# Kernel tuning notes

Hardware: AMD Instinct MI355X
Metric: run time of the kernel (lower is better)

Reference implementation:

```python
import jax, jax.numpy as jnp
import numpy as np

W = 8          # window_size (small/key side)
WU = 2 * W     # window_size_up (big/query side)
H = 4          # num_heads
SF = 128       # sf_dim
BF = 256       # bf_dim
HD = SF // H   # head_dim = 32
SCALE = HD ** -0.5
TABLE = (2 * WU - 1) * (2 * W - 1)  # 465


def _relative_position_index():
    # big coords (2, WU*WU), small coords (2, W*W), 'ij' meshgrid like torch
    ch, cw = jnp.meshgrid(jnp.arange(WU), jnp.arange(WU), indexing='ij')
    big = jnp.stack([ch.reshape(-1), cw.reshape(-1)])          # (2, Nb)
    sh, sw = jnp.meshgrid(jnp.arange(W), jnp.arange(W), indexing='ij')
    small = jnp.stack([sh.reshape(-1), sw.reshape(-1)])        # (2, Ns)
    rel = big[:, :, None] - small[:, None, :]                  # (2, Nb, Ns)
    idx = (rel[0] + W - 1) * (2 * W - 1) + (rel[1] + W - 1)    # (Nb, Ns)
    return idx


def setup_inputs() -> dict:
    key = jax.random.key(0)
    ks = jax.random.split(key, 9)
    B_ = 1024
    Nb, Ns = WU * WU, W * W
    inp = {
        'big_x': jax.random.normal(ks[0], (B_, Nb, BF), jnp.float32),
        'small_x': jax.random.normal(ks[1], (B_, Ns, SF), jnp.float32),
        # proj1: bf_dim -> sf_dim
        'W1': jax.random.normal(ks[2], (BF, SF), jnp.float32) * (BF ** -0.5),
        'b1': jnp.zeros((SF,), jnp.float32),
        # fused qkv: sf_dim -> 3*sf_dim
        'Wqkv': jax.random.normal(ks[3], (SF, 3 * SF), jnp.float32) * (SF ** -0.5),
        'bqkv': jnp.zeros((3 * SF,), jnp.float32),
        # proj2: sf_dim -> bf_dim
        'W2': jax.random.normal(ks[4], (SF, BF), jnp.float32) * (SF ** -0.5),
        'b2': jnp.zeros((BF,), jnp.float32),
        # relative position bias table, trunc_normal std=0.02
        'bias_table': jax.random.normal(ks[5], (TABLE, H), jnp.float32) * 0.02,
    }
    return inp


def reference(big_x, small_x, W1, b1, Wqkv, bqkv, W2, b2, bias_table):
    B_, Nb, _ = big_x.shape
    Ns = small_x.shape[1]

    big = big_x @ W1 + b1                                      # (B, Nb, SF)

    # only q of big and k,v of small are used downstream
    qb = (big @ Wqkv[:, :SF] + bqkv[:SF]).reshape(B_, Nb, H, HD)
    ks_ = (small_x @ Wqkv[:, SF:2 * SF] + bqkv[SF:2 * SF]).reshape(B_, Ns, H, HD)
    vs = (small_x @ Wqkv[:, 2 * SF:] + bqkv[2 * SF:]).reshape(B_, Ns, H, HD)

    attn = jnp.einsum('bqhd,bkhd->bhqk', qb * SCALE, ks_)      # (B, H, Nb, Ns)

    idx = _relative_position_index()                           # (Nb, Ns)
    bias = bias_table[idx]                                     # (Nb, Ns, H)
    attn = attn + jnp.transpose(bias, (2, 0, 1))[None]         # broadcast over B

    attn = jax.nn.softmax(attn, axis=-1)
    out = jnp.einsum('bhqk,bkhd->bqhd', attn, vs).reshape(B_, Nb, SF)
    return out @ W2 + b2                                       # (B, Nb, BF)
```

## Files before the change

kernel.cpp:

```cpp
#include <hip/hip_runtime.h>
#include <stdint.h>

#define NH      4
#define SF      128
#define BF      256
#define HD      32
#define NB      256
#define NS      64
#define NBATCH  1024

typedef short bf16x8 __attribute__((ext_vector_type(8)));
typedef float f32x4  __attribute__((ext_vector_type(4)));

#define WEFFT_OFF 0
#define BEFF_OFF  65536
#define WKVT_OFF  66048
#define W2T_OFF   131584
#define BMATT_OFF 197120
#define KV_OFF    459264
#define WS_NEED   (KV_OFF + (size_t)NBATCH * 32768u)

__device__ __forceinline__ short f2b(float x){
  uint32_t u = __float_as_uint(x);
  u += 0x7fff + ((u >> 16) & 1);
  return (short)(u >> 16);
}
__device__ __forceinline__ uint32_t cvt_pk_bf16(float lo, float hi){
  uint32_t r;
  asm("v_cvt_pk_bf16_f32 %0, %1, %2" : "=v"(r) : "v"(lo), "v"(hi));
  return r;
}
__device__ __forceinline__ int swz256(int row, int byteInRow){
  return row * 256 + (byteInRow ^ ((row & 7) << 4));
}
__device__ __forceinline__ int swz128(int row, int byteInRow){
  return row * 128 + (byteInRow ^ ((row & 7) << 4));
}

__global__ void cowin_prep(const float* __restrict__ W1, const float* __restrict__ b1,
                           const float* __restrict__ Wqkv, const float* __restrict__ bqkv,
                           const float* __restrict__ W2, const float* __restrict__ tbl,
                           void* ws)
{
  short* weffT = (short*)((char*)ws + WEFFT_OFF);
  float* beff  = (float*)((char*)ws + BEFF_OFF);
  short* wkvT  = (short*)((char*)ws + WKVT_OFF);
  short* w2T   = (short*)((char*)ws + W2T_OFF);
  float* bmatT = (float*)((char*)ws + BMATT_OFF);
  const float L2E = 1.4426950408889634f;
  const float QS  = 0.17677669529663687f * L2E;

  int bid = blockIdx.x, t = threadIdx.x;
  if (bid < 128){
    int n = bid, k = t;
    float acc = 0.f;
    for (int c = 0; c < SF; ++c) acc += W1[k * SF + c] * Wqkv[c * (3*SF) + n];
    weffT[n * 256 + k] = f2b(acc * QS);
  } else if (bid == 128){
    if (t < 128){
      int n = t;
      float acc = bqkv[n];
      for (int c = 0; c < SF; ++c) acc += b1[c] * Wqkv[c * (3*SF) + n];
      beff[n] = acc * QS;
    }
  } else if (bid < 145){
    int base = (bid - 129) * 2048 + t * 8;
    for (int j = 0; j < 8; ++j){
      int i = base + j, n = i >> 7, k = i & 127;
      wkvT[i] = f2b(Wqkv[k * (3*SF) + SF + n]);
    }
  } else if (bid < 161){
    int base = (bid - 145) * 2048 + t * 8;
    for (int j = 0; j < 8; ++j){
      int i = base + j, n = i >> 7, k = i & 127;
      w2T[i] = f2b(W2[k * BF + n]);
    }
  } else {
    int i = (bid - 161) * 256 + t;
    int h = i >> 14, q = (i >> 6) & 255, key = i & 63;
    int qh = q >> 4, qw = q & 15, kh = key >> 3, kw = key & 7;
    int idx = (qh - kh + 7) * 15 + (qw - kw + 7);
    bmatT[i] = tbl[idx * 4 + h] * L2E;
  }
}

__global__ __launch_bounds__(256, 4) void cowin_kv(
    const float* __restrict__ small_x, const float* __restrict__ bqkv,
    void* __restrict__ ws)
{
  __shared__ __align__(16) char smem[32768];
  const short* wkvT = (const short*)((const char*)ws + WKVT_OFF);
  char* kvb = (char*)ws + KV_OFF + (size_t)blockIdx.x * 32768;

  const int b = blockIdx.x;
  const int t = threadIdx.x, w = t >> 6, lane = t & 63, li = lane & 15, g = lane >> 4;
  const f32x4 vzero = {0.f, 0.f, 0.f, 0.f};

  {
    int tok = t >> 2, seg = t & 3;
    const float4* src = (const float4*)(small_x + (size_t)b * (NS * SF) + tok * SF + seg * 32);
    float4 v[8];
    #pragma unroll
    for (int i = 0; i < 8; ++i) v[i] = src[i];
    uint32_t pk[16];
    #pragma unroll
    for (int i = 0; i < 8; ++i){
      pk[2*i]   = cvt_pk_bf16(v[i].x, v[i].y);
      pk[2*i+1] = cvt_pk_bf16(v[i].z, v[i].w);
    }
    #pragma unroll
    for (int c = 0; c < 4; ++c){
      uint4 u; u.x = pk[c*4]; u.y = pk[c*4+1]; u.z = pk[c*4+2]; u.w = pk[c*4+3];
      *(uint4*)(smem + swz256(tok, seg * 64 + c * 16)) = u;
    }
  }
  __syncthreads();

  f32x4 acc[4][4];
  #pragma unroll
  for (int m = 0; m < 4; ++m)
    #pragma unroll
    for (int n = 0; n < 4; ++n) acc[m][n] = vzero;

  if (w < 2){
    #pragma unroll
    for (int ks = 0; ks < 4; ++ks){
      bf16x8 a4[4], b4[4];
      #pragma unroll
      for (int mf = 0; mf < 4; ++mf)
        a4[mf] = *(const bf16x8*)(wkvT + (w*64 + mf*16 + li) * 128 + ks*32 + g*8);
      #pragma unroll
      for (int n4 = 0; n4 < 4; ++n4)
        b4[n4] = *(const bf16x8*)(smem + swz256(n4*16 + li, ks*64 + g*16));
      #pragma unroll
      for (int mf = 0; mf < 4; ++mf)
        #pragma unroll
        for (int n4 = 0; n4 < 4; ++n4)
          acc[mf][n4] = __builtin_amdgcn_mfma_f32_16x16x32_bf16(a4[mf], b4[n4], acc[mf][n4], 0, 0, 0);
    }
  } else {
    #pragma unroll
    for (int ks = 0; ks < 4; ++ks){
      bf16x8 a4[4], b4[4];
      #pragma unroll
      for (int m = 0; m < 4; ++m)
        a4[m] = *(const bf16x8*)(smem + swz256(m*16 + li, ks*64 + g*16));
      #pragma unroll
      for (int n4 = 0; n4 < 4; ++n4)
        b4[n4] = *(const bf16x8*)(wkvT + (128 + (w-2)*64 + n4*16 + li) * 128 + ks*32 + g*8);
      #pragma unroll
      for (int m = 0; m < 4; ++m)
        #pragma unroll
        for (int n4 = 0; n4 < 4; ++n4)
          acc[m][n4] = __builtin_amdgcn_mfma_f32_16x16x32_bf16(a4[m], b4[n4], acc[m][n4], 0, 0, 0);
    }
  }
  __syncthreads();

  if (w < 2){
    #pragma unroll
    for (int mf = 0; mf < 4; ++mf){
      int f0 = w*64 + mf*16 + g*4;
      f32x4 bb = *(const f32x4*)(bqkv + SF + f0);
      #pragma unroll
      for (int n4 = 0; n4 < 4; ++n4){
        f32x4 vv = acc[mf][n4];
        uint2 u;
        u.x = cvt_pk_bf16(vv[0] + bb[0], vv[1] + bb[1]);
        u.y = cvt_pk_bf16(vv[2] + bb[2], vv[3] + bb[3]);
        *(uint2*)(smem + swz256(n4*16 + li, f0 * 2)) = u;
      }
    }
  } else {
    #pragma unroll
    for (int n4 = 0; n4 < 4; ++n4){
      int feat = (w-2)*64 + n4*16 + li;
      float bias = bqkv[2*SF + feat];
      #pragma unroll
      for (int m = 0; m < 4; ++m){
        f32x4 vv = acc[m][n4];
        uint2 u;
        u.x = cvt_pk_bf16(vv[0] + bias, vv[1] + bias);
        u.y = cvt_pk_bf16(vv[2] + bias, vv[3] + bias);
        *(uint2*)(smem + 16384 + swz128(feat, (m*16 + g*4) * 2)) = u;
      }
    }
  }
  __syncthreads();

  #pragma unroll
  for (int it = 0; it < 4; ++it){
    int id = it * 256 + t;
    int h = id >> 8, tok = (id >> 2) & 63, c = id & 3;
    uint4 v = *(const uint4*)(smem + swz256(tok, h*64 + c*16));
    *(uint4*)(kvb + id * 16) = v;
  }
  #pragma unroll
  for (int it = 0; it < 4; ++it){
    int id = it * 256 + t;
    int fg = id >> 3, c = id & 7;
    uint4 v = *(const uint4*)(smem + 16384 + swz128(fg, c*16));
    *(uint4*)(kvb + 16384 + id * 16) = v;
  }
}

__global__ __launch_bounds__(256, 4) void cowin_attn(
    const float* __restrict__ big_x, const float* __restrict__ b2,
    const void* __restrict__ ws, float* __restrict__ out)
{
  __shared__ __align__(16) char smem[32768];
  const short* weffT = (const short*)((const char*)ws + WEFFT_OFF);
  const float* beff  = (const float*)((const char*)ws + BEFF_OFF);
  const short* w2T   = (const short*)((const char*)ws + W2T_OFF);
  const float* bmatT = (const float*)((const char*)ws + BMATT_OFF);

  const int b  = blockIdx.x >> 2;
  const int qt = blockIdx.x & 3;
  const char* kvb = (const char*)ws + KV_OFF + (size_t)b * 32768;

  const int t = threadIdx.x, w = t >> 6, lane = t & 63, li = lane & 15, g = lane >> 4;
  const int h = w;
  const f32x4 vzero = {0.f, 0.f, 0.f, 0.f};

  const float* bx = big_x + ((size_t)b * NB + qt * 64) * BF;
  const int qrow = t >> 2, qq = (t & 3) * 16;

  float4 ldA[4], ldB[4];
  {
    const float4* s0 = (const float4*)(bx + qrow * BF + qq);
    #pragma unroll
    for (int i = 0; i < 4; ++i) ldA[i] = s0[i];
    const float4* s1 = (const float4*)(bx + qrow * BF + 64 + qq);
    #pragma unroll
    for (int i = 0; i < 4; ++i) ldB[i] = s1[i];
  }

  auto STAGE = [&](float4* v, char* buf){
    uint32_t pk[8];
    #pragma unroll
    for (int i = 0; i < 4; ++i){
      pk[2*i]   = cvt_pk_bf16(v[i].x, v[i].y);
      pk[2*i+1] = cvt_pk_bf16(v[i].z, v[i].w);
    }
    #pragma unroll
    for (int c = 0; c < 2; ++c){
      uint4 u; u.x = pk[c*4]; u.y = pk[c*4+1]; u.z = pk[c*4+2]; u.w = pk[c*4+3];
      *(uint4*)(buf + swz128(qrow, qq * 2 + c * 16)) = u;
    }
  };
  auto ISSUE = [&](float4* v, int kc){
    const float4* s_ = (const float4*)(bx + qrow * BF + kc * 64 + qq);
    #pragma unroll
    for (int i = 0; i < 4; ++i) v[i] = s_[i];
  };

  f32x4 qacc[2][4];
  #pragma unroll
  for (int mf = 0; mf < 2; ++mf)
    #pragma unroll
    for (int nt = 0; nt < 4; ++nt) qacc[mf][nt] = vzero;

  auto MFMA_D = [&](const char* buf, int kc){
    #pragma unroll
    for (int ks = 0; ks < 2; ++ks){
      bf16x8 a2[2], bq[4];
      #pragma unroll
      for (int mf = 0; mf < 2; ++mf)
        a2[mf] = *(const bf16x8*)(weffT + (w*32 + mf*16 + li) * 256 + kc*64 + ks*32 + g*8);
      #pragma unroll
      for (int nt = 0; nt < 4; ++nt)
        bq[nt] = *(const bf16x8*)(buf + swz128(nt*16 + li, ks*64 + g*16));
      #pragma unroll
      for (int mf = 0; mf < 2; ++mf)
        #pragma unroll
        for (int nt = 0; nt < 4; ++nt)
          qacc[mf][nt] = __builtin_amdgcn_mfma_f32_16x16x32_bf16(a2[mf], bq[nt], qacc[mf][nt], 0, 0, 0);
    }
  };

  char* buf0 = smem;
  char* buf1 = smem + 8192;

  STAGE(ldA, buf0);
  __syncthreads();
  STAGE(ldB, buf1); ISSUE(ldA, 2);
  MFMA_D(buf0, 0);
  __syncthreads();
  STAGE(ldA, buf0); ISSUE(ldB, 3);
  MFMA_D(buf1, 1);
  __syncthreads();
  STAGE(ldB, buf1);
  MFMA_D(buf0, 2);
  __syncthreads();
  MFMA_D(buf1, 3);

  #pragma unroll
  for (int mf = 0; mf < 2; ++mf){
    int f0 = w*32 + mf*16 + g*4;
    f32x4 be = *(const f32x4*)(beff + f0);
    #pragma unroll
    for (int nt = 0; nt < 4; ++nt){
      f32x4 vv = qacc[mf][nt];
      uint2 u;
      u.x = cvt_pk_bf16(vv[0] + be[0], vv[1] + be[1]);
      u.y = cvt_pk_bf16(vv[2] + be[2], vv[3] + be[3]);
      *(uint2*)(smem + 16384 + swz256(nt*16 + li, f0 * 2)) = u;
    }
  }
  __syncthreads();

  f32x4 sacc[4][4];
  #pragma unroll
  for (int m = 0; m < 4; ++m)
    #pragma unroll
    for (int n = 0; n < 4; ++n) sacc[m][n] = vzero;
  {
    bf16x8 afr[4], bfr[4];
    #pragma unroll
    for (int m = 0; m < 4; ++m)
      afr[m] = *(const bf16x8*)(kvb + (h*64 + m*16 + li) * 64 + g*16);
    #pragma unroll
    for (int n = 0; n < 4; ++n)
      bfr[n] = *(const bf16x8*)(smem + 16384 + swz256(n*16 + li, h*64 + g*16));
    #pragma unroll
    for (int m = 0; m < 4; ++m)
      #pragma unroll
      for (int n = 0; n < 4; ++n)
        sacc[m][n] = __builtin_amdgcn_mfma_f32_16x16x32_bf16(afr[m], bfr[n], sacc[m][n], 0, 0, 0);
  }

  #pragma unroll
  for (int n = 0; n < 4; ++n){
    const float* bm = bmatT + ((size_t)(h * 256 + qt*64 + n*16 + li)) * 64;
    #pragma unroll
    for (int m = 0; m < 4; ++m)
      sacc[m][n] += *(const f32x4*)(bm + m*16 + g*4);
  }

  float sm[4];
  #pragma unroll
  for (int n = 0; n < 4; ++n){
    float mx = sacc[0][n][0];
    #pragma unroll
    for (int m = 0; m < 4; ++m)
      #pragma unroll
      for (int r = 0; r < 4; ++r) mx = fmaxf(mx, sacc[m][n][r]);
    mx = fmaxf(mx, __shfl_xor(mx, 16));
    mx = fmaxf(mx, __shfl_xor(mx, 32));
    float s0 = 0.f;
    #pragma unroll
    for (int m = 0; m < 4; ++m)
      #pragma unroll
      for (int r = 0; r < 4; ++r){
        float e = __builtin_amdgcn_exp2f(sacc[m][n][r] - mx);
        sacc[m][n][r] = e;
        s0 += e;
      }
    s0 += __shfl_xor(s0, 16);
    s0 += __shfl_xor(s0, 32);
    sm[n] = __builtin_amdgcn_rcpf(s0);
  }
  __syncthreads();

  char* sp = smem + w * 8192;
  #pragma unroll
  for (int n = 0; n < 4; ++n)
    #pragma unroll
    for (int m = 0; m < 4; ++m){
      uint2 u;
      u.x = cvt_pk_bf16(sacc[m][n][0], sacc[m][n][1]);
      u.y = cvt_pk_bf16(sacc[m][n][2], sacc[m][n][3]);
      *(uint2*)(sp + swz128(n*16 + li, (m*16 + g*4) * 2)) = u;
    }

  f32x4 oacc[2][4];
  #pragma unroll
  for (int m2 = 0; m2 < 2; ++m2)
    #pragma unroll
    for (int n = 0; n < 4; ++n) oacc[m2][n] = vzero;

  #pragma unroll
  for (int kk = 0; kk < 2; ++kk){
    bf16x8 va[2], pb[4];
    #pragma unroll
    for (int m2 = 0; m2 < 2; ++m2)
      va[m2] = *(const bf16x8*)(kvb + 16384 + (h*32 + m2*16 + li) * 128 + kk*64 + g*16);
    #pragma unroll
    for (int n = 0; n < 4; ++n)
      pb[n] = *(const bf16x8*)(sp + swz128(n*16 + li, kk*64 + g*16));
    #pragma unroll
    for (int m2 = 0; m2 < 2; ++m2)
      #pragma unroll
      for (int n = 0; n < 4; ++n)
        oacc[m2][n] = __builtin_amdgcn_mfma_f32_16x16x32_bf16(va[m2], pb[n], oacc[m2][n], 0, 0, 0);
  }
  __syncthreads();

  #pragma unroll
  for (int m2 = 0; m2 < 2; ++m2)
    #pragma unroll
    for (int n = 0; n < 4; ++n){
      float rs = sm[n];
      f32x4 vv = oacc[m2][n];
      uint2 u;
      u.x = cvt_pk_bf16(vv[0] * rs, vv[1] * rs);
      u.y = cvt_pk_bf16(vv[2] * rs, vv[3] * rs);
      *(uint2*)(smem + swz256(n*16 + li, (h*32 + m2*16 + g*4) * 2)) = u;
    }
  __syncthreads();

  float* op = out + ((size_t)b * NB + qt * 64) * BF;
  #pragma unroll
  for (int p = 0; p < 2; ++p){
    f32x4 facc[2][4];
    #pragma unroll
    for (int mo = 0; mo < 2; ++mo)
      #pragma unroll
      for (int nt = 0; nt < 4; ++nt) facc[mo][nt] = vzero;

    #pragma unroll
    for (int kc = 0; kc < 4; ++kc){
      bf16x8 a2[2], b8[4];
      #pragma unroll
      for (int mo = 0; mo < 2; ++mo)
        a2[mo] = *(const bf16x8*)(w2T + (w*64 + p*32 + mo*16 + li) * 128 + kc*32 + g*8);
      #pragma unroll
      for (int nt = 0; nt < 4; ++nt)
        b8[nt] = *(const bf16x8*)(smem + swz256(nt*16 + li, kc*64 + g*16));
      #pragma unroll
      for (int mo = 0; mo < 2; ++mo)
        #pragma unroll
        for (int nt = 0; nt < 4; ++nt)
          facc[mo][nt] = __builtin_amdgcn_mfma_f32_16x16x32_bf16(a2[mo], b8[nt], facc[mo][nt], 0, 0, 0);
    }
    #pragma unroll
    for (int mo = 0; mo < 2; ++mo){
      int c0 = w*64 + p*32 + mo*16 + g*4;
      f32x4 bb = *(const f32x4*)(b2 + c0);
      #pragma unroll
      for (int nt = 0; nt < 4; ++nt){
        f32x4 vv = facc[mo][nt] + bb;
        __builtin_nontemporal_store(vv, (f32x4*)(op + (size_t)(nt*16 + li) * BF + c0));
      }
    }
  }
}

#define LDS_SK  0
#define LDS_SVT 16384
#define LDS_R3  32768
#define LDS_TOTAL 65536

__global__ __launch_bounds__(512, 4) void cowin_main_fb(
    const float* __restrict__ big_x, const float* __restrict__ small_x,
    const float* __restrict__ bqkv,  const float* __restrict__ b2,
    const void* __restrict__ ws, float* __restrict__ out)
{
  extern __shared__ char smem[];
  const short* weffT = (const short*)((const char*)ws + WEFFT_OFF);
  const float* beff  = (const float*)((const char*)ws + BEFF_OFF);
  const short* wkvT  = (const short*)((const char*)ws + WKVT_OFF);
  const short* w2T   = (const short*)((const char*)ws + W2T_OFF);
  const float* bmatT = (const float*)((const char*)ws + BMATT_OFF);

  const int bid = blockIdx.x;
  const int b  = bid >> 1;
  const int hf = bid & 1;
  const int t    = threadIdx.x;
  const int w    = t >> 6;
  const int lane = t & 63;
  const int li   = lane & 15;
  const int g    = lane >> 4;
  const int h  = w & 3;
  const int qh = w >> 2;

  const f32x4 vzero = {0.f, 0.f, 0.f, 0.f};
  const int tok = t >> 3, p = t & 7;
  const int qrow = t >> 1, qq = (t & 1) * 32;

  const float* bx = big_x + (size_t)b * NB * BF + (size_t)hf * 128 * BF;

  float4 ld[4];
  {
    const float* sx = small_x + (size_t)b * (NS * SF);
    const float4* s0 = (const float4*)(sx + tok * SF + p * 16);
    float4 sv[4];
    #pragma unroll
    for (int i = 0; i < 4; ++i) sv[i] = s0[i];
    const float4* s1 = (const float4*)(bx + qrow * BF + qq);
    float4 bv[8];
    #pragma unroll
    for (int i = 0; i < 8; ++i) bv[i] = s1[i];
    uint32_t pk[8];
    #pragma unroll
    for (int i = 0; i < 4; ++i){
      pk[2*i]   = cvt_pk_bf16(sv[i].x, sv[i].y);
      pk[2*i+1] = cvt_pk_bf16(sv[i].z, sv[i].w);
    }
    #pragma unroll
    for (int c = 0; c < 2; ++c){
      uint4 u; u.x = pk[c*4]; u.y = pk[c*4+1]; u.z = pk[c*4+2]; u.w = pk[c*4+3];
      *(uint4*)(smem + LDS_SK + swz256(tok, p * 32 + c * 16)) = u;
    }
    uint32_t pk2[16];
    #pragma unroll
    for (int i = 0; i < 8; ++i){
      pk2[2*i]   = cvt_pk_bf16(bv[i].x, bv[i].y);
      pk2[2*i+1] = cvt_pk_bf16(bv[i].z, bv[i].w);
    }
    #pragma unroll
    for (int c = 0; c < 4; ++c){
      uint4 u; u.x = pk2[c*4]; u.y = pk2[c*4+1]; u.z = pk2[c*4+2]; u.w = pk2[c*4+3];
      *(uint4*)(smem + LDS_R3 + swz128(qrow, qq * 2 + c * 16)) = u;
    }
    const float4* s2 = (const float4*)(bx + qrow * BF + 64 + qq);
    #pragma unroll
    for (int i = 0; i < 4; ++i) ld[i] = s2[i];
  }
  __syncthreads();

  f32x4 kv8[8];
  #pragma unroll
  for (int i = 0; i < 8; ++i) kv8[i] = vzero;
  if (w < 4){
    #pragma unroll
    for (int ks = 0; ks < 4; ++ks){
      bf16x8 a2[2];
      #pragma unroll
      for (int mf = 0; mf < 2; ++mf)
        a2[mf] = *(const bf16x8*)(wkvT + (w*32 + mf*16 + li) * 128 + ks*32 + g*8);
      #pragma unroll
      for (int n4 = 0; n4 < 4; ++n4){
        bf16x8 b4 = *(const bf16x8*)(smem + LDS_SK + swz256(n4*16 + li, (ks*32 + g*8) * 2));
        #pragma unroll
        for (int mf = 0; mf < 2; ++mf)
          kv8[mf*4+n4] = __builtin_amdgcn_mfma_f32_16x16x32_bf16(a2[mf], b4, kv8[mf*4+n4], 0, 0, 0);
      }
    }
  } else {
    #pragma unroll
    for (int ks = 0; ks < 4; ++ks){
      bf16x8 afr[4];
      #pragma unroll
      for (int m = 0; m < 4; ++m)
        afr[m] = *(const bf16x8*)(smem + LDS_SK + swz256(m*16 + li, (ks*32 + g*8) * 2));
      #pragma unroll
      for (int n2 = 0; n2 < 2; ++n2){
        int n = w * 32 + n2 * 16 + li;
        bf16x8 bfr = *(const bf16x8*)(wkvT + n * 128 + ks*32 + g*8);
        #pragma unroll
        for (int m = 0; m < 4; ++m)
          kv8[m*2+n2] = __builtin_amdgcn_mfma_f32_16x16x32_bf16(afr[m], bfr, kv8[m*2+n2], 0, 0, 0);
      }
    }
  }
  __syncthreads();

  if (w < 4){
    #pragma unroll
    for (int mf = 0; mf < 2; ++mf){
      int f0 = w*32 + mf*16 + g*4;
      f32x4 bb = *(const f32x4*)(bqkv + SF + f0);
      #pragma unroll
      for (int n4 = 0; n4 < 4; ++n4){
        f32x4 vv = kv8[mf*4+n4];
        uint2 u;
        u.x = cvt_pk_bf16(vv[0] + bb[0], vv[1] + bb[1]);
        u.y = cvt_pk_bf16(vv[2] + bb[2], vv[3] + bb[3]);
        *(uint2*)(smem + LDS_SK + swz256(n4*16 + li, f0 * 2)) = u;
      }
    }
  } else {
    #pragma unroll
    for (int n2 = 0; n2 < 2; ++n2){
      int feat = (w-4)*32 + n2*16 + li;
      float bias = bqkv[2*SF + feat];
      #pragma unroll
      for (int m = 0; m < 4; ++m){
        f32x4 vv = kv8[m*2+n2];
        uint2 u;
        u.x = cvt_pk_bf16(vv[0] + bias, vv[1] + bias);
        u.y = cvt_pk_bf16(vv[2] + bias, vv[3] + bias);
        *(uint2*)(smem + LDS_SVT + swz128(feat, (m*16 + g*4) * 2)) = u;
      }
    }
  }

  f32x4 qacc[8];
  #pragma unroll
  for (int m = 0; m < 8; ++m) qacc[m] = vzero;
  for (int kc = 0; kc < 4; ++kc){
    __syncthreads();
    if (kc < 3){
      uint32_t pk[16];
      #pragma unroll
      for (int i = 0; i < 4; ++i){
        pk[2*i]   = cvt_pk_bf16(ld[i].x, ld[i].y);
        pk[2*i+1] = cvt_pk_bf16(ld[i].z, ld[i].w);
      }
      char* bufn = smem + LDS_R3 + ((kc + 1) & 1) * 16384;
      #pragma unroll
      for (int c = 0; c < 2; ++c){
        uint4 u; u.x = pk[c*4]; u.y = pk[c*4+1]; u.z = pk[c*4+2]; u.w = pk[c*4+3];
        *(uint4*)(bufn + swz128(qrow, qq * 2 + c * 16)) = u;
      }
      if (kc < 2){
        const float4* s_ = (const float4*)(bx + qrow * BF + (kc + 2) * 64 + qq);
        #pragma unroll
        for (int i = 0; i < 4; ++i) ld[i] = s_[i];
      }
    }
    const char* buf = smem + LDS_R3 + (kc & 1) * 16384;
    #pragma unroll
    for (int ks = 0; ks < 2; ++ks){
      bf16x8 a = *(const bf16x8*)(weffT + (w*16 + li) * 256 + kc*64 + ks*32 + g*8);
      #pragma unroll
      for (int nt = 0; nt < 8; ++nt){
        bf16x8 bq = *(const bf16x8*)(buf + swz128(nt*16 + li, (ks*32 + g*8) * 2));
        qacc[nt] = __builtin_amdgcn_mfma_f32_16x16x32_bf16(a, bq, qacc[nt], 0, 0, 0);
      }
    }
  }
  __syncthreads();

  {
    f32x4 be = *(const f32x4*)(beff + w*16 + g*4);
    #pragma unroll
    for (int nt = 0; nt < 8; ++nt){
      f32x4 vv = qacc[nt];
      uint2 u;
      u.x = cvt_pk_bf16(vv[0] + be[0], vv[1] + be[1]);
      u.y = cvt_pk_bf16(vv[2] + be[2], vv[3] + be[3]);
      *(uint2*)(smem + LDS_R3 + swz256(nt*16 + li, (w*16 + g*4) * 2)) = u;
    }
  }
  __syncthreads();

  f32x4 sacc[4][4];
  #pragma unroll
  for (int m = 0; m < 4; ++m)
    #pragma unroll
    for (int n = 0; n < 4; ++n) sacc[m][n] = vzero;
  {
    bf16x8 afr[4];
    #pragma unroll
    for (int m = 0; m < 4; ++m)
      afr[m] = *(const bf16x8*)(smem + LDS_SK + swz256(m*16 + li, (h*32 + g*8) * 2));
    #pragma unroll
    for (int n = 0; n < 4; ++n){
      bf16x8 bfr = *(const bf16x8*)(smem + LDS_R3 + swz256(qh*64 + n*16 + li, (h*32 + g*8) * 2));
      #pragma unroll
      for (int m = 0; m < 4; ++m)
        sacc[m][n] = __builtin_amdgcn_mfma_f32_16x16x32_bf16(afr[m], bfr, sacc[m][n], 0, 0, 0);
    }
  }
  __syncthreads();

  #pragma unroll
  for (int n = 0; n < 4; ++n){
    const float* bm = bmatT + ((size_t)(h * 256 + hf*128 + qh*64 + n*16 + li)) * 64;
    #pragma unroll
    for (int m = 0; m < 4; ++m)
      sacc[m][n] += *(const f32x4*)(bm + m*16 + g*4);
  }

  float sm[4];
  #pragma unroll
  for (int n = 0; n < 4; ++n){
    float mx = sacc[0][n][0];
    #pragma unroll
    for (int m = 0; m < 4; ++m)
      #pragma unroll
      for (int r = 0; r < 4; ++r) mx = fmaxf(mx, sacc[m][n][r]);
    mx = fmaxf(mx, __shfl_xor(mx, 16));
    mx = fmaxf(mx, __shfl_xor(mx, 32));
    float s0 = 0.f;
    #pragma unroll
    for (int m = 0; m < 4; ++m)
      #pragma unroll
      for (int r = 0; r < 4; ++r){
        float e = __builtin_amdgcn_exp2f(sacc[m][n][r] - mx);
        sacc[m][n][r] = e;
        s0 += e;
      }
    s0 += __shfl_xor(s0, 16);
    s0 += __shfl_xor(s0, 32);
    sm[n] = __builtin_amdgcn_rcpf(s0);
  }

  f32x4 oacc[2][2][2];
  #pragma unroll
  for (int hl = 0; hl < 2; ++hl)
    #pragma unroll
    for (int m2 = 0; m2 < 2; ++m2)
      #pragma unroll
      for (int n4 = 0; n4 < 2; ++n4) oacc[hl][m2][n4] = vzero;

  char* sp = smem + LDS_R3 + w * 4096;
  #pragma unroll
  for (int hl = 0; hl < 2; ++hl){
    #pragma unroll
    for (int n4 = 0; n4 < 2; ++n4){
      int n = hl * 2 + n4;
      #pragma unroll
      for (int m = 0; m < 4; ++m){
        uint2 u;
        u.x = cvt_pk_bf16(sacc[m][n][0], sacc[m][n][1]);
        u.y = cvt_pk_bf16(sacc[m][n][2], sacc[m][n][3]);
        *(uint2*)(sp + swz128(n4 * 16 + li, (m * 16 + g * 4) * 2)) = u;
      }
    }
    #pragma unroll
    for (int kk = 0; kk < 2; ++kk){
      bf16x8 afr2[2];
      #pragma unroll
      for (int m2 = 0; m2 < 2; ++m2)
        afr2[m2] = *(const bf16x8*)(smem + LDS_SVT + swz128(h*32 + m2*16 + li, (kk*32 + g*8) * 2));
      #pragma unroll
      for (int n4 = 0; n4 < 2; ++n4){
        bf16x8 bfr = *(const bf16x8*)(sp + swz128(n4 * 16 + li, (kk*32 + g*8) * 2));
        #pragma unroll
        for (int m2 = 0; m2 < 2; ++m2)
          oacc[hl][m2][n4] = __builtin_amdgcn_mfma_f32_16x16x32_bf16(afr2[m2], bfr, oacc[hl][m2][n4], 0, 0, 0);
      }
    }
  }
  __syncthreads();

  #pragma unroll
  for (int hl = 0; hl < 2; ++hl)
    #pragma unroll
    for (int m2 = 0; m2 < 2; ++m2)
      #pragma unroll
      for (int n4 = 0; n4 < 2; ++n4){
        float rs = sm[hl * 2 + n4];
        f32x4 vv = oacc[hl][m2][n4];
        uint2 u;
        u.x = cvt_pk_bf16(vv[0] * rs, vv[1] * rs);
        u.y = cvt_pk_bf16(vv[2] * rs, vv[3] * rs);
        int q = qh * 64 + hl * 32 + n4 * 16 + li;
        *(uint2*)(smem + LDS_R3 + swz256(q, (h*32 + m2*16 + g*4) * 2)) = u;
      }
  __syncthreads();

  f32x4 facc[2][8];
  #pragma unroll
  for (int mo = 0; mo < 2; ++mo)
    #pragma unroll
    for (int nt = 0; nt < 8; ++nt) facc[mo][nt] = vzero;

  #pragma unroll
  for (int kc = 0; kc < 4; ++kc){
    bf16x8 a2[2];
    #pragma unroll
    for (int mo = 0; mo < 2; ++mo)
      a2[mo] = *(const bf16x8*)(w2T + (w*32 + mo*16 + li) * 128 + kc*32 + g*8);
    #pragma unroll
    for (int nt = 0; nt < 8; ++nt){
      bf16x8 b8 = *(const bf16x8*)(smem + LDS_R3 + swz256(nt*16 + li, (kc*32 + g*8) * 2));
      #pragma unroll
      for (int mo = 0; mo < 2; ++mo)
        facc[mo][nt] = __builtin_amdgcn_mfma_f32_16x16x32_bf16(a2[mo], b8, facc[mo][nt], 0, 0, 0);
    }
  }

  float* op = out + (size_t)b * NB * BF + (size_t)hf * 128 * BF;
  #pragma unroll
  for (int mo = 0; mo < 2; ++mo){
    int c0 = w*32 + mo*16 + g*4;
    f32x4 bb = *(const f32x4*)(b2 + c0);
    #pragma unroll
    for (int nt = 0; nt < 8; ++nt){
      f32x4 vv = facc[mo][nt] + bb;
      *(f32x4*)(op + (size_t)(nt*16 + li) * BF + c0) = vv;
    }
  }
}

extern "C" void kernel_launch(void* const* d_in, const int* in_sizes, int n_in,
                              void* d_out, int out_size, void* d_ws, size_t ws_size,
                              hipStream_t stream)
{
  const float* big_x   = (const float*)d_in[0];
  const float* small_x = (const float*)d_in[1];
  const float* W1      = (const float*)d_in[2];
  const float* b1      = (const float*)d_in[3];
  const float* Wqkv    = (const float*)d_in[4];
  const float* bqkv    = (const float*)d_in[5];
  const float* W2      = (const float*)d_in[6];
  const float* b2      = (const float*)d_in[7];
  const float* tbl     = (const float*)d_in[8];
  float* out = (float*)d_out;

  (void)in_sizes; (void)n_in; (void)out_size;

  cowin_prep<<<417, 256, 0, stream>>>(W1, b1, Wqkv, bqkv, W2, tbl, d_ws);

  if (ws_size >= WS_NEED){
    cowin_kv<<<NBATCH, 256, 0, stream>>>(small_x, bqkv, d_ws);
    cowin_attn<<<NBATCH * 4, 256, 0, stream>>>(big_x, b2, d_ws, out);
  } else {
    hipFuncSetAttribute(reinterpret_cast<const void*>(cowin_main_fb),
                        hipFuncAttributeMaxDynamicSharedMemorySize, LDS_TOTAL);
    cowin_main_fb<<<NBATCH * 2, 512, LDS_TOTAL, stream>>>(big_x, small_x, bqkv, b2, d_ws, out);
  }
}
```

Baseline: 208.2 us.

## Halve attention query tile to 32 rows and load big_x in one shot

The attention kernel now handles 32 query rows per block instead of 64, doubling the grid and cutting per-block LDS to 24 KB and register tiles in half, with launch bounds raised to 6 blocks per CU. The double-buffered staged load of big_x is replaced by a single bulk load of the whole 32x256 tile into a 512-byte-row swizzled LDS buffer, followed by one barrier. One barrier is dropped by placing the attention output in a separate LDS region. The aim is higher occupancy and less sync overhead, at the cost of re-reading K/V, weights and the bias matrix twice as often per batch and losing the load/compute overlap.

```diff
diff --git a/kernel.cpp b/kernel.cpp
--- a/kernel.cpp
+++ b/kernel.cpp
@@ -30,11 +30,14 @@
   asm("v_cvt_pk_bf16_f32 %0, %1, %2" : "=v"(r) : "v"(lo), "v"(hi));
   return r;
 }
+__device__ __forceinline__ int swz128(int row, int byteInRow){
+  return row * 128 + (byteInRow ^ ((row & 7) << 4));
+}
 __device__ __forceinline__ int swz256(int row, int byteInRow){
   return row * 256 + (byteInRow ^ ((row & 7) << 4));
 }
-__device__ __forceinline__ int swz128(int row, int byteInRow){
-  return row * 128 + (byteInRow ^ ((row & 7) << 4));
+__device__ __forceinline__ int swz512(int row, int byteInRow){
+  return row * 512 + (byteInRow ^ ((row & 7) << 4));
 }
 
 __global__ void cowin_prep(const float* __restrict__ W1, const float* __restrict__ b1,
@@ -204,102 +207,75 @@
   }
 }
 
-__global__ __launch_bounds__(256, 4) void cowin_attn(
+__global__ __launch_bounds__(256, 6) void cowin_attn(
     const float* __restrict__ big_x, const float* __restrict__ b2,
     const void* __restrict__ ws, float* __restrict__ out)
 {
-  __shared__ __align__(16) char smem[32768];
+  __shared__ __align__(16) char smem[24576];
   const short* weffT = (const short*)((const char*)ws + WEFFT_OFF);
   const float* beff  = (const float*)((const char*)ws + BEFF_OFF);
   const short* w2T   = (const short*)((const char*)ws + W2T_OFF);
   const float* bmatT = (const float*)((const char*)ws + BMATT_OFF);
 
-  const int b  = blockIdx.x >> 2;
-  const int qt = blockIdx.x & 3;
+  const int b  = blockIdx.x >> 3;
+  const int qt = blockIdx.x & 7;
   const char* kvb = (const char*)ws + KV_OFF + (size_t)b * 32768;
 
   const int t = threadIdx.x, w = t >> 6, lane = t & 63, li = lane & 15, g = lane >> 4;
   const int h = w;
   const f32x4 vzero = {0.f, 0.f, 0.f, 0.f};
 
-  const float* bx = big_x + ((size_t)b * NB + qt * 64) * BF;
-  const int qrow = t >> 2, qq = (t & 3) * 16;
-
-  float4 ldA[4], ldB[4];
+  const float* bx = big_x + ((size_t)b * NB + qt * 32) * BF;
+
   {
-    const float4* s0 = (const float4*)(bx + qrow * BF + qq);
-    #pragma unroll
-    for (int i = 0; i < 4; ++i) ldA[i] = s0[i];
-    const float4* s1 = (const float4*)(bx + qrow * BF + 64 + qq);
-    #pragma unroll
-    for (int i = 0; i < 4; ++i) ldB[i] = s1[i];
-  }
-
-  auto STAGE = [&](float4* v, char* buf){
-    uint32_t pk[8];
-    #pragma unroll
-    for (int i = 0; i < 4; ++i){
+    const int row = t >> 3, c0 = (t & 7);
+    const float4* src = (const float4*)(bx + row * BF + c0 * 32);
+    float4 v[8];
+    #pragma unroll
+    for (int i = 0; i < 8; ++i) v[i] = src[i];
+    uint32_t pk[16];
+    #pragma unroll
+    for (int i = 0; i < 8; ++i){
       pk[2*i]   = cvt_pk_bf16(v[i].x, v[i].y);
       pk[2*i+1] = cvt_pk_bf16(v[i].z, v[i].w);
     }
     #pragma unroll
-    for (int c = 0; c < 2; ++c){
+    for (int c = 0; c < 4; ++c){
       uint4 u; u.x = pk[c*4]; u.y = pk[c*4+1]; u.z = pk[c*4+2]; u.w = pk[c*4+3];
-      *(uint4*)(buf + swz128(qrow, qq * 2 + c * 16)) = u;
-    }
-  };
-  auto ISSUE = [&](float4* v, int kc){
-    const float4* s_ = (const float4*)(bx + qrow * BF + kc * 64 + qq);
-    #pragma unroll
-    for (int i = 0; i < 4; ++i) v[i] = s_[i];
-  };
-
-  f32x4 qacc[2][4];
-  #pragma unroll
-  for (int mf = 0; mf < 2; ++mf)
-    #pragma unroll
-    for (int nt = 0; nt < 4; ++nt) qacc[mf][nt] = vzero;
-
-  auto MFMA_D = [&](const char* buf, int kc){
+      *(uint4*)(smem + swz512(row, c0 * 64 + c * 16)) = u;
+    }
+  }
+  __syncthreads();
+
+  f32x4 qacc[2][2];
+  #pragma unroll
+  for (int mf = 0; mf < 2; ++mf){ qacc[mf][0] = vzero; qacc[mf][1] = vzero; }
+
+  #pragma unroll
+  for (int kc = 0; kc < 4; ++kc){
     #pragma unroll
     for (int ks = 0; ks < 2; ++ks){
-      bf16x8 a2[2], bq[4];
+      bf16x8 a2[2], bq[2];
       #pragma unroll
       for (int mf = 0; mf < 2; ++mf)
         a2[mf] = *(const bf16x8*)(weffT + (w*32 + mf*16 + li) * 256 + kc*64 + ks*32 + g*8);
       #pragma unroll
-      for (int nt = 0; nt < 4; ++nt)
-        bq[nt] = *(const bf16x8*)(buf + swz128(nt*16 + li, ks*64 + g*16));
+      for (int nt = 0; nt < 2; ++nt)
+        bq[nt] = *(const bf16x8*)(smem + swz512(nt*16 + li, kc*128 + ks*64 + g*16));
       #pragma unroll
       for (int mf = 0; mf < 2; ++mf)
         #pragma unroll
-        for (int nt = 0; nt < 4; ++nt)
+        for (int nt = 0; nt < 2; ++nt)
           qacc[mf][nt] = __builtin_amdgcn_mfma_f32_16x16x32_bf16(a2[mf], bq[nt], qacc[mf][nt], 0, 0, 0);
     }
-  };
-
-  char* buf0 = smem;
-  char* buf1 = smem + 8192;
-
-  STAGE(ldA, buf0);
-  __syncthreads();
-  STAGE(ldB, buf1); ISSUE(ldA, 2);
-  MFMA_D(buf0, 0);
-  __syncthreads();
-  STAGE(ldA, buf0); ISSUE(ldB, 3);
-  MFMA_D(buf1, 1);
-  __syncthreads();
-  STAGE(ldB, buf1);
-  MFMA_D(buf0, 2);
-  __syncthreads();
-  MFMA_D(buf1, 3);
+  }
 
   #pragma unroll
   for (int mf = 0; mf < 2; ++mf){
     int f0 = w*32 + mf*16 + g*4;
     f32x4 be = *(const f32x4*)(beff + f0);
     #pragma unroll
-    for (int nt = 0; nt < 4; ++nt){
+    for (int nt = 0; nt < 2; ++nt){
       f32x4 vv = qacc[mf][nt];
       uint2 u;
       u.x = cvt_pk_bf16(vv[0] + be[0], vv[1] + be[1]);
@@ -309,37 +285,35 @@
   }
   __syncthreads();
 
-  f32x4 sacc[4][4];
-  #pragma unroll
-  for (int m = 0; m < 4; ++m)
-    #pragma unroll
-    for (int n = 0; n < 4; ++n) sacc[m][n] = vzero;
+  f32x4 sacc[4][2];
+  #pragma unroll
+  for (int m = 0; m < 4; ++m){ sacc[m][0] = vzero; sacc[m][1] = vzero; }
   {
-    bf16x8 afr[4], bfr[4];
+    bf16x8 afr[4], bfr[2];
     #pragma unroll
     for (int m = 0; m < 4; ++m)
       afr[m] = *(const bf16x8*)(kvb + (h*64 + m*16 + li) * 64 + g*16);
     #pragma unroll
-    for (int n = 0; n < 4; ++n)
+    for (int n = 0; n < 2; ++n)
       bfr[n] = *(const bf16x8*)(smem + 16384 + swz256(n*16 + li, h*64 + g*16));
     #pragma unroll
     for (int m = 0; m < 4; ++m)
       #pragma unroll
-      for (int n = 0; n < 4; ++n)
+      for (int n = 0; n < 2; ++n)
         sacc[m][n] = __builtin_amdgcn_mfma_f32_16x16x32_bf16(afr[m], bfr[n], sacc[m][n], 0, 0, 0);
   }
 
   #pragma unroll
-  for (int n = 0; n < 4; ++n){
-    const float* bm = bmatT + ((size_t)(h * 256 + qt*64 + n*16 + li)) * 64;
+  for (int n = 0; n < 2; ++n){
+    const float* bm = bmatT + ((size_t)(h * 256 + qt*32 + n*16 + li)) * 64;
     #pragma unroll
     for (int m = 0; m < 4; ++m)
       sacc[m][n] += *(const f32x4*)(bm + m*16 + g*4);
   }
 
-  float sm[4];
-  #pragma unroll
-  for (int n = 0; n < 4; ++n){
+  float sm[2];
+  #pragma unroll
+  for (int n = 0; n < 2; ++n){
     float mx = sacc[0][n][0];
     #pragma unroll
     for (int m = 0; m < 4; ++m)
@@ -362,75 +336,70 @@
   }
   __syncthreads();
 
-  char* sp = smem + w * 8192;
-  #pragma unroll
-  for (int n = 0; n < 4; ++n)
+  char* sp = smem + w * 4096;
+  #pragma unroll
+  for (int n = 0; n < 2; ++n)
     #pragma unroll
     for (int m = 0; m < 4; ++m){
       uint2 u;
       u.x = cvt_pk_bf16(sacc[m][n][0], sacc[m][n][1]);
       u.y = cvt_pk_bf16(sacc[m][n][2], sacc[m][n][3]);
-      *(uint2*)(sp + swz128(n*16 + li, (m*16 + g*4) * 2)) = u;
-    }
-
-  f32x4 oacc[2][4];
-  #pragma unroll
-  for (int m2 = 0; m2 < 2; ++m2)
-    #pragma unroll
-    for (int n = 0; n < 4; ++n) oacc[m2][n] = vzero;
+      *(uint2*)(sp + swz128(n*16 + li, m*32 + g*8)) = u;
+    }
+
+  f32x4 oacc[2][2];
+  #pragma unroll
+  for (int m2 = 0; m2 < 2; ++m2){ oacc[m2][0] = vzero; oacc[m2][1] = vzero; }
 
   #pragma unroll
   for (int kk = 0; kk < 2; ++kk){
-    bf16x8 va[2], pb[4];
+    bf16x8 va[2], pb[2];
     #pragma unroll
     for (int m2 = 0; m2 < 2; ++m2)
       va[m2] = *(const bf16x8*)(kvb + 16384 + (h*32 + m2*16 + li) * 128 + kk*64 + g*16);
     #pragma unroll
-    for (int n = 0; n < 4; ++n)
+    for (int n = 0; n < 2; ++n)
       pb[n] = *(const bf16x8*)(sp + swz128(n*16 + li, kk*64 + g*16));
     #pragma unroll
     for (int m2 = 0; m2 < 2; ++m2)
       #pragma unroll
-      for (int n = 0; n < 4; ++n)
+      for (int n = 0; n < 2; ++n)
         oacc[m2][n] = __builtin_amdgcn_mfma_f32_16x16x32_bf16(va[m2], pb[n], oacc[m2][n], 0, 0, 0);
   }
-  __syncthreads();
 
   #pragma unroll
   for (int m2 = 0; m2 < 2; ++m2)
     #pragma unroll
-    for (int n = 0; n < 4; ++n){
+    for (int n = 0; n < 2; ++n){
       float rs = sm[n];
       f32x4 vv = oacc[m2][n];
       uint2 u;
       u.x = cvt_pk_bf16(vv[0] * rs, vv[1] * rs);
       u.y = cvt_pk_bf16(vv[2] * rs, vv[3] * rs);
-      *(uint2*)(smem + swz256(n*16 + li, (h*32 + m2*16 + g*4) * 2)) = u;
-    }
-  __syncthreads();
-
-  float* op = out + ((size_t)b * NB + qt * 64) * BF;
+      *(uint2*)(smem + 16384 + swz256(n*16 + li, (h*32 + m2*16 + g*4) * 2)) = u;
+    }
+  __syncthreads();
+
+  float* op = out + ((size_t)b * NB + qt * 32) * BF;
   #pragma unroll
   for (int p = 0; p < 2; ++p){
-    f32x4 facc[2][4];
-    #pragma unroll
-    for (int mo = 0; mo < 2; ++mo)
-      #pragma unroll
-      for (int nt = 0; nt < 4; ++nt) facc[mo][nt] = vzero;
+    f32x4 facc[2][2];
+    #pragma unroll
+    for (int mo = 0; mo < 2; ++mo){ facc[mo][0] = vzero; facc[mo][1] = vzero; }
 
     #pragma unroll
     for (int kc = 0; kc < 4; ++kc){
-      bf16x8 a2[2], b8[4];
+      bf16x8 a2[2], b8[2];
       #pragma unroll
       for (int mo = 0; mo < 2; ++mo)
         a2[mo] = *(const bf16x8*)(w2T + (w*64 + p*32 + mo*16 + li) * 128 + kc*32 + g*8);
       #pragma unroll
-      for (int nt = 0; nt < 4; ++nt)
-        b8[nt] = *(const bf16x8*)(smem + swz256(nt*16 + li, kc*64 + g*16));
+      for (int nt = 0; nt < 2; ++nt)
+        b8[nt] = *(const bf16x8*)(smem + 16384 + swz256(nt*16 + li, kc*64 + g*16));
       #pragma unroll
       for (int mo = 0; mo < 2; ++mo)
         #pragma unroll
-        for (int nt = 0; nt < 4; ++nt)
+        for (int nt = 0; nt < 2; ++nt)
           facc[mo][nt] = __builtin_amdgcn_mfma_f32_16x16x32_bf16(a2[mo], b8[nt], facc[mo][nt], 0, 0, 0);
     }
     #pragma unroll
@@ -438,7 +407,7 @@
       int c0 = w*64 + p*32 + mo*16 + g*4;
       f32x4 bb = *(const f32x4*)(b2 + c0);
       #pragma unroll
-      for (int nt = 0; nt < 4; ++nt){
+      for (int nt = 0; nt < 2; ++nt){
         f32x4 vv = facc[mo][nt] + bb;
         __builtin_nontemporal_store(vv, (f32x4*)(op + (size_t)(nt*16 + li) * BF + c0));
       }
@@ -798,7 +767,7 @@
 
   if (ws_size >= WS_NEED){
     cowin_kv<<<NBATCH, 256, 0, stream>>>(small_x, bqkv, d_ws);
-    cowin_attn<<<NBATCH * 4, 256, 0, stream>>>(big_x, b2, d_ws, out);
+    cowin_attn<<<NBATCH * 8, 256, 0, stream>>>(big_x, b2, d_ws, out);
   } else {
     hipFuncSetAttribute(reinterpret_cast<const void*>(cowin_main_fb),
                         hipFuncAttributeMaxDynamicSharedMemorySize, LDS_TOTAL);
```

Result: slower. 287.7 us (+38.2%).

## Load big_x fragments directly from global, prefetch K/V fragments, raise occupancy

Applied to the files above, without the earlier changes.

Drops the LDS double-buffered staging of the big_x tile with its barriers. Each wave now reads its own MFMA B-operand rows of big_x straight from global memory and converts them to bf16 in registers. K and V fragments are loaded into registers at kernel start to overlap their latency with the first GEMM. The launch bounds target 5 blocks per SM instead of 4. The cost is redundant global reads: all four waves read the same big_x tile, and the 32-byte per-lane row accesses coalesce less well. The extra live registers may also spill under the tighter occupancy bound.

```diff
diff --git a/kernel.cpp b/kernel.cpp
--- a/kernel.cpp
+++ b/kernel.cpp
@@ -30,11 +30,19 @@
   asm("v_cvt_pk_bf16_f32 %0, %1, %2" : "=v"(r) : "v"(lo), "v"(hi));
   return r;
 }
+__device__ __forceinline__ bf16x8 cvt8(float4 a, float4 b){
+  union { uint32_t u[4]; bf16x8 v; } x;
+  x.u[0] = cvt_pk_bf16(a.x, a.y);
+  x.u[1] = cvt_pk_bf16(a.z, a.w);
+  x.u[2] = cvt_pk_bf16(b.x, b.y);
+  x.u[3] = cvt_pk_bf16(b.z, b.w);
+  return x.v;
+}
+__device__ __forceinline__ int swz128(int row, int byteInRow){
+  return row * 128 + (byteInRow ^ ((row & 7) << 4));
+}
 __device__ __forceinline__ int swz256(int row, int byteInRow){
   return row * 256 + (byteInRow ^ ((row & 7) << 4));
-}
-__device__ __forceinline__ int swz128(int row, int byteInRow){
-  return row * 128 + (byteInRow ^ ((row & 7) << 4));
 }
 
 __global__ void cowin_prep(const float* __restrict__ W1, const float* __restrict__ b1,
@@ -204,7 +212,7 @@
   }
 }
 
-__global__ __launch_bounds__(256, 4) void cowin_attn(
+__global__ __launch_bounds__(256, 5) void cowin_attn(
     const float* __restrict__ big_x, const float* __restrict__ b2,
     const void* __restrict__ ws, float* __restrict__ out)
 {
@@ -223,36 +231,16 @@
   const f32x4 vzero = {0.f, 0.f, 0.f, 0.f};
 
   const float* bx = big_x + ((size_t)b * NB + qt * 64) * BF;
-  const int qrow = t >> 2, qq = (t & 3) * 16;
-
-  float4 ldA[4], ldB[4];
-  {
-    const float4* s0 = (const float4*)(bx + qrow * BF + qq);
-    #pragma unroll
-    for (int i = 0; i < 4; ++i) ldA[i] = s0[i];
-    const float4* s1 = (const float4*)(bx + qrow * BF + 64 + qq);
-    #pragma unroll
-    for (int i = 0; i < 4; ++i) ldB[i] = s1[i];
-  }
-
-  auto STAGE = [&](float4* v, char* buf){
-    uint32_t pk[8];
-    #pragma unroll
-    for (int i = 0; i < 4; ++i){
-      pk[2*i]   = cvt_pk_bf16(v[i].x, v[i].y);
-      pk[2*i+1] = cvt_pk_bf16(v[i].z, v[i].w);
-    }
-    #pragma unroll
-    for (int c = 0; c < 2; ++c){
-      uint4 u; u.x = pk[c*4]; u.y = pk[c*4+1]; u.z = pk[c*4+2]; u.w = pk[c*4+3];
-      *(uint4*)(buf + swz128(qrow, qq * 2 + c * 16)) = u;
-    }
-  };
-  auto ISSUE = [&](float4* v, int kc){
-    const float4* s_ = (const float4*)(bx + qrow * BF + kc * 64 + qq);
-    #pragma unroll
-    for (int i = 0; i < 4; ++i) v[i] = s_[i];
-  };
+
+  bf16x8 kfr[4], vfr[2][2];
+  #pragma unroll
+  for (int m = 0; m < 4; ++m)
+    kfr[m] = *(const bf16x8*)(kvb + (h*64 + m*16 + li) * 64 + g*16);
+  #pragma unroll
+  for (int kk = 0; kk < 2; ++kk)
+    #pragma unroll
+    for (int m2 = 0; m2 < 2; ++m2)
+      vfr[kk][m2] = *(const bf16x8*)(kvb + 16384 + (h*32 + m2*16 + li) * 128 + kk*64 + g*16);
 
   f32x4 qacc[2][4];
   #pragma unroll
@@ -260,7 +248,8 @@
     #pragma unroll
     for (int nt = 0; nt < 4; ++nt) qacc[mf][nt] = vzero;
 
-  auto MFMA_D = [&](const char* buf, int kc){
+  #pragma unroll
+  for (int kc = 0; kc < 4; ++kc){
     #pragma unroll
     for (int ks = 0; ks < 2; ++ks){
       bf16x8 a2[2], bq[4];
@@ -268,31 +257,19 @@
       for (int mf = 0; mf < 2; ++mf)
         a2[mf] = *(const bf16x8*)(weffT + (w*32 + mf*16 + li) * 256 + kc*64 + ks*32 + g*8);
       #pragma unroll
-      for (int nt = 0; nt < 4; ++nt)
-        bq[nt] = *(const bf16x8*)(buf + swz128(nt*16 + li, ks*64 + g*16));
+      for (int nt = 0; nt < 4; ++nt){
+        const float* rp = bx + (size_t)(nt*16 + li) * BF + kc*64 + ks*32 + g*8;
+        float4 v0 = *(const float4*)rp;
+        float4 v1 = *(const float4*)(rp + 4);
+        bq[nt] = cvt8(v0, v1);
+      }
       #pragma unroll
       for (int mf = 0; mf < 2; ++mf)
         #pragma unroll
         for (int nt = 0; nt < 4; ++nt)
           qacc[mf][nt] = __builtin_amdgcn_mfma_f32_16x16x32_bf16(a2[mf], bq[nt], qacc[mf][nt], 0, 0, 0);
     }
-  };
-
-  char* buf0 = smem;
-  char* buf1 = smem + 8192;
-
-  STAGE(ldA, buf0);
-  __syncthreads();
-  STAGE(ldB, buf1); ISSUE(ldA, 2);
-  MFMA_D(buf0, 0);
-  __syncthreads();
-  STAGE(ldA, buf0); ISSUE(ldB, 3);
-  MFMA_D(buf1, 1);
-  __syncthreads();
-  STAGE(ldB, buf1);
-  MFMA_D(buf0, 2);
-  __syncthreads();
-  MFMA_D(buf1, 3);
+  }
 
   #pragma unroll
   for (int mf = 0; mf < 2; ++mf){
@@ -304,7 +281,7 @@
       uint2 u;
       u.x = cvt_pk_bf16(vv[0] + be[0], vv[1] + be[1]);
       u.y = cvt_pk_bf16(vv[2] + be[2], vv[3] + be[3]);
-      *(uint2*)(smem + 16384 + swz256(nt*16 + li, f0 * 2)) = u;
+      *(uint2*)(smem + swz256(nt*16 + li, f0 * 2)) = u;
     }
   }
   __syncthreads();
@@ -315,18 +292,15 @@
     #pragma unroll
     for (int n = 0; n < 4; ++n) sacc[m][n] = vzero;
   {
-    bf16x8 afr[4], bfr[4];
+    bf16x8 bfr[4];
+    #pragma unroll
+    for (int n = 0; n < 4; ++n)
+      bfr[n] = *(const bf16x8*)(smem + swz256(n*16 + li, h*64 + g*16));
     #pragma unroll
     for (int m = 0; m < 4; ++m)
-      afr[m] = *(const bf16x8*)(kvb + (h*64 + m*16 + li) * 64 + g*16);
-    #pragma unroll
-    for (int n = 0; n < 4; ++n)
-      bfr[n] = *(const bf16x8*)(smem + 16384 + swz256(n*16 + li, h*64 + g*16));
-    #pragma unroll
-    for (int m = 0; m < 4; ++m)
       #pragma unroll
       for (int n = 0; n < 4; ++n)
-        sacc[m][n] = __builtin_amdgcn_mfma_f32_16x16x32_bf16(afr[m], bfr[n], sacc[m][n], 0, 0, 0);
+        sacc[m][n] = __builtin_amdgcn_mfma_f32_16x16x32_bf16(kfr[m], bfr[n], sacc[m][n], 0, 0, 0);
   }
 
   #pragma unroll
@@ -370,7 +344,7 @@
       uint2 u;
       u.x = cvt_pk_bf16(sacc[m][n][0], sacc[m][n][1]);
       u.y = cvt_pk_bf16(sacc[m][n][2], sacc[m][n][3]);
-      *(uint2*)(sp + swz128(n*16 + li, (m*16 + g*4) * 2)) = u;
+      *(uint2*)(sp + swz128(n*16 + li, m*32 + g*8)) = u;
     }
 
   f32x4 oacc[2][4];
@@ -381,10 +355,7 @@
 
   #pragma unroll
   for (int kk = 0; kk < 2; ++kk){
-    bf16x8 va[2], pb[4];
-    #pragma unroll
-    for (int m2 = 0; m2 < 2; ++m2)
-      va[m2] = *(const bf16x8*)(kvb + 16384 + (h*32 + m2*16 + li) * 128 + kk*64 + g*16);
+    bf16x8 pb[4];
     #pragma unroll
     for (int n = 0; n < 4; ++n)
       pb[n] = *(const bf16x8*)(sp + swz128(n*16 + li, kk*64 + g*16));
@@ -392,7 +363,7 @@
     for (int m2 = 0; m2 < 2; ++m2)
       #pragma unroll
       for (int n = 0; n < 4; ++n)
-        oacc[m2][n] = __builtin_amdgcn_mfma_f32_16x16x32_bf16(va[m2], pb[n], oacc[m2][n], 0, 0, 0);
+        oacc[m2][n] = __builtin_amdgcn_mfma_f32_16x16x32_bf16(vfr[kk][m2], pb[n], oacc[m2][n], 0, 0, 0);
   }
   __syncthreads();
 
```

After: 324.7 us. +56.0%, slower.

## Split fused attention kernel into separate Q-projection GEMM and attention kernels

Applied to the files above, without the earlier changes.

Splits the fused attention kernel in two. A new Q-projection kernel writes bf16 Q to a global workspace buffer, and a second kernel reads it back to run attention and the output projection. The aim is to lower LDS and register pressure so each kernel can keep more blocks resident, and to preload K/V fragments into registers. The cost is an extra 64 MB bf16 round trip through global memory plus a second launch. It also needs a larger workspace, and if that is missing it takes the fallback path.

```diff
diff --git a/kernel.cpp b/kernel.cpp
--- a/kernel.cpp
+++ b/kernel.cpp
@@ -18,7 +18,8 @@
 #define W2T_OFF   131584
 #define BMATT_OFF 197120
 #define KV_OFF    459264
-#define WS_NEED   (KV_OFF + (size_t)NBATCH * 32768u)
+#define QWS_OFF   (KV_OFF + (size_t)NBATCH * 32768u)
+#define WS_NEED2  (QWS_OFF + (size_t)NBATCH * 256u * 128u * 2u)
 
 __device__ __forceinline__ short f2b(float x){
   uint32_t u = __float_as_uint(x);
@@ -30,11 +31,11 @@
   asm("v_cvt_pk_bf16_f32 %0, %1, %2" : "=v"(r) : "v"(lo), "v"(hi));
   return r;
 }
+__device__ __forceinline__ int swz128(int row, int byteInRow){
+  return row * 128 + (byteInRow ^ ((row & 7) << 4));
+}
 __device__ __forceinline__ int swz256(int row, int byteInRow){
   return row * 256 + (byteInRow ^ ((row & 7) << 4));
-}
-__device__ __forceinline__ int swz128(int row, int byteInRow){
-  return row * 128 + (byteInRow ^ ((row & 7) << 4));
 }
 
 __global__ void cowin_prep(const float* __restrict__ W1, const float* __restrict__ b1,
@@ -204,25 +205,19 @@
   }
 }
 
-__global__ __launch_bounds__(256, 4) void cowin_attn(
-    const float* __restrict__ big_x, const float* __restrict__ b2,
-    const void* __restrict__ ws, float* __restrict__ out)
+__global__ __launch_bounds__(256, 8) void cowin_qgemm(
+    const float* __restrict__ big_x, const void* __restrict__ ws,
+    short* __restrict__ qws)
 {
-  __shared__ __align__(16) char smem[32768];
+  __shared__ __align__(16) char smem[16384];
   const short* weffT = (const short*)((const char*)ws + WEFFT_OFF);
   const float* beff  = (const float*)((const char*)ws + BEFF_OFF);
-  const short* w2T   = (const short*)((const char*)ws + W2T_OFF);
-  const float* bmatT = (const float*)((const char*)ws + BMATT_OFF);
-
-  const int b  = blockIdx.x >> 2;
-  const int qt = blockIdx.x & 3;
-  const char* kvb = (const char*)ws + KV_OFF + (size_t)b * 32768;
-
+
+  const int bid = blockIdx.x;
   const int t = threadIdx.x, w = t >> 6, lane = t & 63, li = lane & 15, g = lane >> 4;
-  const int h = w;
   const f32x4 vzero = {0.f, 0.f, 0.f, 0.f};
 
-  const float* bx = big_x + ((size_t)b * NB + qt * 64) * BF;
+  const float* bx = big_x + (size_t)bid * 64 * BF;
   const int qrow = t >> 2, qq = (t & 3) * 16;
 
   float4 ldA[4], ldB[4];
@@ -294,6 +289,7 @@
   __syncthreads();
   MFMA_D(buf1, 3);
 
+  short* qp = qws + (size_t)bid * 64 * 128;
   #pragma unroll
   for (int mf = 0; mf < 2; ++mf){
     int f0 = w*32 + mf*16 + g*4;
@@ -304,10 +300,38 @@
       uint2 u;
       u.x = cvt_pk_bf16(vv[0] + be[0], vv[1] + be[1]);
       u.y = cvt_pk_bf16(vv[2] + be[2], vv[3] + be[3]);
-      *(uint2*)(smem + 16384 + swz256(nt*16 + li, f0 * 2)) = u;
-    }
-  }
-  __syncthreads();
+      *(uint2*)(qp + (size_t)(nt*16 + li) * 128 + f0) = u;
+    }
+  }
+}
+
+__global__ __launch_bounds__(256, 5) void cowin_attn2(
+    const float* __restrict__ b2, const void* __restrict__ ws,
+    float* __restrict__ out)
+{
+  __shared__ __align__(16) char smem[32768];
+  const short* w2T   = (const short*)((const char*)ws + W2T_OFF);
+  const float* bmatT = (const float*)((const char*)ws + BMATT_OFF);
+
+  const int bid = blockIdx.x;
+  const int b  = bid >> 2;
+  const int qt = bid & 3;
+  const char* kvb = (const char*)ws + KV_OFF + (size_t)b * 32768;
+  const short* qp = (const short*)((const char*)ws + QWS_OFF) + (size_t)bid * 64 * 128;
+
+  const int t = threadIdx.x, w = t >> 6, lane = t & 63, li = lane & 15, g = lane >> 4;
+  const int h = w;
+  const f32x4 vzero = {0.f, 0.f, 0.f, 0.f};
+
+  bf16x8 kfr[4], vfr[2][2];
+  #pragma unroll
+  for (int m = 0; m < 4; ++m)
+    kfr[m] = *(const bf16x8*)(kvb + (h*64 + m*16 + li) * 64 + g*16);
+  #pragma unroll
+  for (int kk = 0; kk < 2; ++kk)
+    #pragma unroll
+    for (int m2 = 0; m2 < 2; ++m2)
+      vfr[kk][m2] = *(const bf16x8*)(kvb + 16384 + (h*32 + m2*16 + li) * 128 + kk*64 + g*16);
 
   f32x4 sacc[4][4];
   #pragma unroll
@@ -315,18 +339,15 @@
     #pragma unroll
     for (int n = 0; n < 4; ++n) sacc[m][n] = vzero;
   {
-    bf16x8 afr[4], bfr[4];
+    bf16x8 bfr[4];
+    #pragma unroll
+    for (int n = 0; n < 4; ++n)
+      bfr[n] = *(const bf16x8*)(qp + (size_t)(n*16 + li) * 128 + h*32 + g*8);
     #pragma unroll
     for (int m = 0; m < 4; ++m)
-      afr[m] = *(const bf16x8*)(kvb + (h*64 + m*16 + li) * 64 + g*16);
-    #pragma unroll
-    for (int n = 0; n < 4; ++n)
-      bfr[n] = *(const bf16x8*)(smem + 16384 + swz256(n*16 + li, h*64 + g*16));
-    #pragma unroll
-    for (int m = 0; m < 4; ++m)
       #pragma unroll
       for (int n = 0; n < 4; ++n)
-        sacc[m][n] = __builtin_amdgcn_mfma_f32_16x16x32_bf16(afr[m], bfr[n], sacc[m][n], 0, 0, 0);
+        sacc[m][n] = __builtin_amdgcn_mfma_f32_16x16x32_bf16(kfr[m], bfr[n], sacc[m][n], 0, 0, 0);
   }
 
   #pragma unroll
@@ -360,7 +381,6 @@
     s0 += __shfl_xor(s0, 32);
     sm[n] = __builtin_amdgcn_rcpf(s0);
   }
-  __syncthreads();
 
   char* sp = smem + w * 8192;
   #pragma unroll
@@ -370,7 +390,7 @@
       uint2 u;
       u.x = cvt_pk_bf16(sacc[m][n][0], sacc[m][n][1]);
       u.y = cvt_pk_bf16(sacc[m][n][2], sacc[m][n][3]);
-      *(uint2*)(sp + swz128(n*16 + li, (m*16 + g*4) * 2)) = u;
+      *(uint2*)(sp + swz128(n*16 + li, m*32 + g*8)) = u;
     }
 
   f32x4 oacc[2][4];
@@ -381,10 +401,7 @@
 
   #pragma unroll
   for (int kk = 0; kk < 2; ++kk){
-    bf16x8 va[2], pb[4];
-    #pragma unroll
-    for (int m2 = 0; m2 < 2; ++m2)
-      va[m2] = *(const bf16x8*)(kvb + 16384 + (h*32 + m2*16 + li) * 128 + kk*64 + g*16);
+    bf16x8 pb[4];
     #pragma unroll
     for (int n = 0; n < 4; ++n)
       pb[n] = *(const bf16x8*)(sp + swz128(n*16 + li, kk*64 + g*16));
@@ -392,7 +409,7 @@
     for (int m2 = 0; m2 < 2; ++m2)
       #pragma unroll
       for (int n = 0; n < 4; ++n)
-        oacc[m2][n] = __builtin_amdgcn_mfma_f32_16x16x32_bf16(va[m2], pb[n], oacc[m2][n], 0, 0, 0);
+        oacc[m2][n] = __builtin_amdgcn_mfma_f32_16x16x32_bf16(vfr[kk][m2], pb[n], oacc[m2][n], 0, 0, 0);
   }
   __syncthreads();
 
@@ -409,7 +426,7 @@
     }
   __syncthreads();
 
-  float* op = out + ((size_t)b * NB + qt * 64) * BF;
+  float* op = out + (size_t)bid * 64 * BF;
   #pragma unroll
   for (int p = 0; p < 2; ++p){
     f32x4 facc[2][4];
@@ -796,9 +813,11 @@
 
   cowin_prep<<<417, 256, 0, stream>>>(W1, b1, Wqkv, bqkv, W2, tbl, d_ws);
 
-  if (ws_size >= WS_NEED){
+  if (ws_size >= WS_NEED2){
     cowin_kv<<<NBATCH, 256, 0, stream>>>(small_x, bqkv, d_ws);
-    cowin_attn<<<NBATCH * 4, 256, 0, stream>>>(big_x, b2, d_ws, out);
+    cowin_qgemm<<<NBATCH * 4, 256, 0, stream>>>(
+        big_x, d_ws, (short*)((char*)d_ws + QWS_OFF));
+    cowin_attn2<<<NBATCH * 4, 256, 0, stream>>>(b2, d_ws, out);
   } else {
     hipFuncSetAttribute(reinterpret_cast<const void*>(cowin_main_fb),
                         hipFuncAttributeMaxDynamicSharedMemorySize, LDS_TOTAL);
```

Result: slower. 340.3 us (+63.5%).
